# Kernel optimization log

Hardware: AMD Instinct MI355X
Metric: run time of the kernel (lower is better)

Reference implementation:

```python
import jax, jax.numpy as jnp
import numpy as np
import math

HID, NH, NKV, HD = 2048, 16, 4, 128
GROUPS = NH // NKV

def fq(x, bits, axis=None):
    # symmetric fake-quant with straight-through rounding; per-tensor unless axis given
    qmax = 2.0 ** (bits - 1) - 1.0
    if axis is None:
        amax = jnp.max(jnp.abs(x))
    else:
        amax = jnp.max(jnp.abs(x), axis=axis, keepdims=True)
    scale = jnp.maximum(amax, 1e-8) / qmax
    q = jnp.clip(jnp.round(x / scale), -qmax - 1.0, qmax) * scale
    return x + jax.lax.stop_gradient(q - x)

def dyn_quant_linear(x, W, b, w_bits=8):
    # DynamicQuantLinear: per-out-channel weight fake-quant + dynamic per-tensor 8-bit act quant
    Wq = fq(W, w_bits, axis=1)          # W: [out, in]
    xq = fq(x, 8)
    y = xq @ Wq.T
    return y + b if b is not None else y

def fq_matmul(a, b, a_bits, b_bits):
    # FakeQuantMatmul
    return jnp.einsum('hqd,hdk->hqk', fq(a, a_bits), fq(b, b_bits))

def rotate_half(x):
    x1, x2 = jnp.split(x, 2, axis=-1)
    return jnp.concatenate([-x2, x1], axis=-1)

def setup_inputs() -> dict:
    key = jax.random.key(0)
    ks = jax.random.split(key, 12)
    inp = {
        'hidden_states': jax.random.normal(ks[0], (1, 512, HID), jnp.float32),
        'cos': jax.random.uniform(ks[1], (1, 512, HD), jnp.float32),
        'sin': jax.random.uniform(ks[2], (1, 512, HD), jnp.float32),
        'cache_k': jax.random.normal(ks[3], (NKV, 8192, HD), jnp.float32),
        'cache_v': jax.random.normal(ks[4], (NKV, 8192, HD), jnp.float32),
        'mask': jnp.zeros((1, 512, 8192), jnp.float32),
        'Wq': jax.random.normal(ks[5], (NH * HD, HID), jnp.float32) * 0.02,
        'bq': jnp.zeros((NH * HD,), jnp.float32),
        'Wk': jax.random.normal(ks[6], (NKV * HD, HID), jnp.float32) * 0.02,
        'bk': jnp.zeros((NKV * HD,), jnp.float32),
        'Wv': jax.random.normal(ks[7], (NKV * HD, HID), jnp.float32) * 0.02,
        'bv': jnp.zeros((NKV * HD,), jnp.float32),
        'Wo': jax.random.normal(ks[8], (HID, NH * HD), jnp.float32) * 0.02,
    }
    return inp

def reference(hidden_states, cos, sin, cache_k, cache_v, mask, Wq, bq, Wk, bk, Wv, bv, Wo):
    # ConstFakeQuant on incoming caches
    cache_k = fq(cache_k, 8)
    cache_v = fq(cache_v, 8)
    seqlen = hidden_states.shape[1]
    x = hidden_states.reshape(seqlen, HID)  # batch_size == 1
    q = dyn_quant_linear(x, Wq, bq).reshape(seqlen, NH, HD).transpose(1, 0, 2)    # [NH,S,D]
    k = dyn_quant_linear(x, Wk, bk).reshape(seqlen, NKV, HD).transpose(1, 0, 2)   # [NKV,S,D]
    v = dyn_quant_linear(x, Wv, bv).reshape(seqlen, NKV, HD).transpose(1, 0, 2)   # [NKV,S,D]
    # RoPE
    q = q * cos + rotate_half(q) * sin
    k = k * cos + rotate_half(k) * sin
    c_len = cache_k.shape[1]
    # sliding KV cache: drop oldest seqlen, append new
    cache_k = jnp.concatenate([cache_k[:, seqlen:, :], k], axis=1)   # [NKV,c_len,D]
    cache_v = jnp.concatenate([cache_v[:, seqlen:, :], v], axis=1)
    kT = cache_k.transpose(0, 2, 1)                                   # [NKV,D,c_len]
    q4 = q.reshape(NKV, GROUPS * seqlen, HD)
    attn = fq_matmul(q4, kT, 8, 8)                                    # [NKV,G*S,c_len]
    attn = attn.reshape(NH, seqlen, c_len) / math.sqrt(HD)
    attn = attn + mask
    attn = jax.nn.softmax(attn, axis=-1)
    attn = attn.reshape(NKV, GROUPS * seqlen, c_len)
    out = fq_matmul(attn, cache_v, 8, 8)                              # sv: [NKV,G*S,D]
    out = out.reshape(NH, seqlen, HD).transpose(1, 0, 2).reshape(1, seqlen, HID)
    out = dyn_quant_linear(out.reshape(seqlen, HID), Wo, None).reshape(1, seqlen, HID)
    # cache outputs re-fake-quantized
    k_out = fq(k, 8)
    v_out = fq(v, 8)
    return (out, k_out, v_out)
```

## Files before the change

kernel.cpp:

```cpp
#include <hip/hip_runtime.h>
#include <math.h>

#define S_LEN 512
#define HID 2048
#define NH 16
#define NKV 4
#define HD 128
#define CL 8192
#define TAILN (CL - S_LEN)
#define KS1 16
#define KCH1 (CL / KS1)
#define KS2 8
#define KCH2 (CL / KS2)
#define INV_SQRT_HD 0.08838834764831845f

typedef unsigned short u16;
typedef __attribute__((ext_vector_type(8))) unsigned short u16x8;
typedef __attribute__((ext_vector_type(4))) unsigned short u16x4;
typedef __attribute__((ext_vector_type(8))) short bf16x8;
typedef __attribute__((ext_vector_type(4))) float f32x4;

enum {
  SC_AMAX_X = 0, SC_AMAX_CK, SC_AMAX_CK_TAIL, SC_AMAX_CV, SC_AMAX_CV_TAIL,
  SC_AMAX_Q, SC_AMAX_K, SC_AMAX_V, SC_AMAX_AO, SC_MIN_L,
  SC_NUM
};

__device__ __forceinline__ float warpMax64(float v) {
  #pragma unroll
  for (int o = 32; o; o >>= 1) v = fmaxf(v, __shfl_down(v, o, 64));
  return v;
}
__device__ __forceinline__ float warpMin64(float v) {
  #pragma unroll
  for (int o = 32; o; o >>= 1) v = fminf(v, __shfl_down(v, o, 64));
  return v;
}
__device__ __forceinline__ float blockMax256(float v) {
  __shared__ float sm_[4];
  __syncthreads();
  v = warpMax64(v);
  if ((threadIdx.x & 63) == 0) sm_[threadIdx.x >> 6] = v;
  __syncthreads();
  return fmaxf(fmaxf(sm_[0], sm_[1]), fmaxf(sm_[2], sm_[3]));
}
__device__ __forceinline__ float blockMin256(float v) {
  __shared__ float sn_[4];
  __syncthreads();
  v = warpMin64(v);
  if ((threadIdx.x & 63) == 0) sn_[threadIdx.x >> 6] = v;
  __syncthreads();
  return fminf(fminf(sn_[0], sn_[1]), fminf(sn_[2], sn_[3]));
}
__device__ __forceinline__ void atomicMinPosF(float* a, float v) {
  atomicMin((unsigned int*)a, __float_as_uint(v));
}
__device__ __forceinline__ float clampq(float q) {
  return fminf(fmaxf(q, -128.f), 127.f);
}
__device__ __forceinline__ u16 bf16bits(float f) {
  return (u16)(__float_as_uint(f) >> 16);
}
__device__ __forceinline__ float mk_scale(float am) {
  return fmaxf(am, 1e-8f) / 127.f;
}
__device__ __forceinline__ void gl2lds16(const u16* g, u16* l) {
  __builtin_amdgcn_global_load_lds((const __attribute__((address_space(1))) void*)g,
                                   (__attribute__((address_space(3))) void*)l, 16, 0, 0);
}

__global__ void k_init(float* sc) {
  int i = threadIdx.x;
  if (i < SC_NUM) sc[i] = (i == SC_MIN_L) ? INFINITY : 0.f;
}

__global__ __launch_bounds__(256) void k_absmax_part(const float* __restrict__ x, int n4,
                                                     float* __restrict__ pp) {
  float m = 0.f;
  const float4* x4 = (const float4*)x;
  for (int i = blockIdx.x * 256 + threadIdx.x; i < n4; i += gridDim.x * 256) {
    float4 v = x4[i];
    m = fmaxf(m, fmaxf(fmaxf(fabsf(v.x), fabsf(v.y)), fmaxf(fabsf(v.z), fabsf(v.w))));
  }
  m = blockMax256(m);
  if (threadIdx.x == 0) pp[blockIdx.x] = m;
}

__global__ __launch_bounds__(256) void k_absmax_caches_part(const float* __restrict__ ck,
                                                            const float* __restrict__ cv,
                                                            float* __restrict__ pp) {
  const int n4 = NKV * CL * HD / 4;
  float mkf = 0.f, mkt = 0.f, mvf = 0.f, mvt = 0.f;
  for (int i = blockIdx.x * 256 + threadIdx.x; i < 2 * n4; i += gridDim.x * 256) {
    int isv = i >= n4;
    int j = i - isv * n4;
    float4 v = ((const float4*)(isv ? cv : ck))[j];
    float a = fmaxf(fmaxf(fabsf(v.x), fabsf(v.y)), fmaxf(fabsf(v.z), fabsf(v.w)));
    int t = (j >> 5) & (CL - 1);
    if (isv) { mvf = fmaxf(mvf, a); if (t >= S_LEN) mvt = fmaxf(mvt, a); }
    else     { mkf = fmaxf(mkf, a); if (t >= S_LEN) mkt = fmaxf(mkt, a); }
  }
  mkf = blockMax256(mkf); mkt = blockMax256(mkt);
  mvf = blockMax256(mvf); mvt = blockMax256(mvt);
  if (threadIdx.x == 0) {
    pp[512 + blockIdx.x] = mkf;
    pp[1024 + blockIdx.x] = mkt;
    pp[1536 + blockIdx.x] = mvf;
    pp[2048 + blockIdx.x] = mvt;
  }
}

__global__ __launch_bounds__(256) void k_reduce_pre(const float* __restrict__ pp, float* __restrict__ sc) {
  const int slots[5] = {SC_AMAX_X, SC_AMAX_CK, SC_AMAX_CK_TAIL, SC_AMAX_CV, SC_AMAX_CV_TAIL};
  #pragma unroll
  for (int r = 0; r < 5; r++) {
    float v = fmaxf(pp[r * 512 + threadIdx.x], pp[r * 512 + 256 + threadIdx.x]);
    v = blockMax256(v);
    if (threadIdx.x == 0) sc[slots[r]] = v;
  }
}

__global__ __launch_bounds__(256) void k_quant_w_all(const float* __restrict__ Wq, const float* __restrict__ Wk,
                                                     const float* __restrict__ Wv, const float* __restrict__ Wo,
                                                     u16* __restrict__ WQb, u16* __restrict__ WKb,
                                                     u16* __restrict__ WVb, u16* __restrict__ WOb,
                                                     float* __restrict__ SWq, float* __restrict__ SWk,
                                                     float* __restrict__ SWv, float* __restrict__ SWo) {
  int r = blockIdx.x;
  const float* W; u16* Wb; float* SW; int row;
  if (r < 2048)      { W = Wq; Wb = WQb; SW = SWq; row = r; }
  else if (r < 2560) { W = Wk; Wb = WKb; SW = SWk; row = r - 2048; }
  else if (r < 3072) { W = Wv; Wb = WVb; SW = SWv; row = r - 2560; }
  else               { W = Wo; Wb = WOb; SW = SWo; row = r - 3072; }
  size_t base = (size_t)row * HID;
  const float4* w4 = (const float4*)(W + base);
  const int n4 = HID / 4;
  float am = 0.f;
  for (int i = threadIdx.x; i < n4; i += 256) {
    float4 v = w4[i];
    am = fmaxf(am, fmaxf(fmaxf(fabsf(v.x), fabsf(v.y)), fmaxf(fabsf(v.z), fabsf(v.w))));
  }
  am = blockMax256(am);
  float s = fmaxf(am, 1e-8f) / 127.f;
  if (threadIdx.x == 0) SW[row] = s;
  for (int i = threadIdx.x; i < n4; i += 256) {
    float4 v = w4[i];
    u16x4 o;
    o[0] = bf16bits(clampq(rintf(v.x / s)));
    o[1] = bf16bits(clampq(rintf(v.y / s)));
    o[2] = bf16bits(clampq(rintf(v.z / s)));
    o[3] = bf16bits(clampq(rintf(v.w / s)));
    *(u16x4*)(Wb + base + (size_t)i * 4) = o;
  }
}

__global__ __launch_bounds__(256) void k_quant_act_b(const float* __restrict__ in, u16* __restrict__ outp,
                                                     int n4, const float* __restrict__ sc, int axslot) {
  float s = mk_scale(sc[axslot]);
  const float4* i4 = (const float4*)in;
  for (int i = blockIdx.x * 256 + threadIdx.x; i < n4; i += gridDim.x * 256) {
    float4 v = i4[i];
    u16x4 o;
    o[0] = bf16bits(clampq(rintf(v.x / s)));
    o[1] = bf16bits(clampq(rintf(v.y / s)));
    o[2] = bf16bits(clampq(rintf(v.z / s)));
    o[3] = bf16bits(clampq(rintf(v.w / s)));
    *(u16x4*)(outp + (size_t)i * 4) = o;
  }
}

__global__ __launch_bounds__(256) void k_quant_q(const float* __restrict__ QB, u16* __restrict__ QI,
                                                 const float* __restrict__ sc) {
  int idx = blockIdx.x * 256 + threadIdx.x;
  float s = mk_scale(sc[SC_AMAX_Q]);
  int e = idx * 4;
  int srow = e >> 11, rem = e & 2047;
  int h = rem >> 7, d = rem & 127;
  float4 v = *(const float4*)&QB[e];
  u16x4 o;
  o[0] = bf16bits(clampq(rintf(v.x / s)));
  o[1] = bf16bits(clampq(rintf(v.y / s)));
  o[2] = bf16bits(clampq(rintf(v.z / s)));
  o[3] = bf16bits(clampq(rintf(v.w / s)));
  *(u16x4*)(QI + ((size_t)h * S_LEN + srow) * HD + d) = o;
}

__global__ __launch_bounds__(256) void k_gemm_qkv(const u16* __restrict__ A,
                                                  const u16* __restrict__ WQb, const u16* __restrict__ WKb,
                                                  const u16* __restrict__ WVb,
                                                  const float* __restrict__ SWq, const float* __restrict__ SWk,
                                                  const float* __restrict__ SWv,
                                                  const float* __restrict__ bq, const float* __restrict__ bk,
                                                  const float* __restrict__ bv,
                                                  const float* __restrict__ sc,
                                                  float* __restrict__ QB, float* __restrict__ KB,
                                                  float* __restrict__ VB) {
  __shared__ u16 Al[64 * 64];
  __shared__ u16 Bl[64 * 64];
  int bx = blockIdx.x;
  const u16* B; const float* SW; const float* bias; float* C; int N, c0;
  if (bx < 32)      { B = WQb; SW = SWq; bias = bq; C = QB; N = HID; c0 = bx * 64; }
  else if (bx < 40) { B = WKb; SW = SWk; bias = bk; C = KB; N = NKV * HD; c0 = (bx - 32) * 64; }
  else              { B = WVb; SW = SWv; bias = bv; C = VB; N = NKV * HD; c0 = (bx - 40) * 64; }
  int tid = threadIdx.x, lane = tid & 63, w = tid >> 6;
  int g = lane >> 4, c = lane & 15;
  int wy = w >> 1, wx = w & 1;
  int r0 = blockIdx.y * 64;
  float sx = mk_scale(sc[SC_AMAX_X]);
  f32x4 acc[2][2] = {};
  for (int k0 = 0; k0 < HID; k0 += 64) {
    __syncthreads();
    #pragma unroll
    for (int i = 0; i < 2; i++) {
      int b = tid + i * 256;
      int row = b >> 3, c8d = b & 7, c8s = c8d ^ (row & 7);
      gl2lds16(A + (size_t)(r0 + row) * HID + k0 + c8s * 8, Al + b * 8);
    }
    #pragma unroll
    for (int i = 0; i < 2; i++) {
      int b = tid + i * 256;
      int row = b >> 3, c8d = b & 7, c8s = c8d ^ (row & 7);
      gl2lds16(B + (size_t)(c0 + row) * HID + k0 + c8s * 8, Bl + b * 8);
    }
    __syncthreads();
    #pragma unroll
    for (int ks = 0; ks < 2; ks++) {
      bf16x8 af[2], bf[2];
      #pragma unroll
      for (int a = 0; a < 2; a++) {
        int row = wy * 32 + a * 16 + c;
        af[a] = *(const bf16x8*)(Al + row * 64 + (((4 * ks + g) ^ (row & 7)) * 8));
      }
      #pragma unroll
      for (int b = 0; b < 2; b++) {
        int row = wx * 32 + b * 16 + c;
        bf[b] = *(const bf16x8*)(Bl + row * 64 + (((4 * ks + g) ^ (row & 7)) * 8));
      }
      #pragma unroll
      for (int a = 0; a < 2; a++)
        #pragma unroll
        for (int b = 0; b < 2; b++)
          acc[a][b] = __builtin_amdgcn_mfma_f32_16x16x32_bf16(af[a], bf[b], acc[a][b], 0, 0, 0);
    }
  }
  #pragma unroll
  for (int a = 0; a < 2; a++)
    #pragma unroll
    for (int b = 0; b < 2; b++) {
      int col = c0 + wx * 32 + b * 16 + c;
      float sca = sx * SW[col];
      float bs = bias[col];
      #pragma unroll
      for (int r = 0; r < 4; r++) {
        int row = r0 + wy * 32 + a * 16 + 4 * g + r;
        C[(size_t)row * N + col] = acc[a][b][r] * sca + bs;
      }
    }
}

__global__ __launch_bounds__(256) void k_gemm_q(const u16* __restrict__ A, const u16* __restrict__ B,
                                                const float* __restrict__ SW, const float* __restrict__ sc,
                                                int axslot, float* __restrict__ C, int M, int N, int K) {
  __shared__ u16 Al[64 * 64];
  __shared__ u16 Bl[64 * 64];
  int tid = threadIdx.x, lane = tid & 63, w = tid >> 6;
  int g = lane >> 4, c = lane & 15;
  int wy = w >> 1, wx = w & 1;
  int r0 = blockIdx.y * 64, c0 = blockIdx.x * 64;
  float sx = mk_scale(sc[axslot]);
  f32x4 acc[2][2] = {};
  for (int k0 = 0; k0 < K; k0 += 64) {
    __syncthreads();
    #pragma unroll
    for (int i = 0; i < 2; i++) {
      int b = tid + i * 256;
      int row = b >> 3, c8d = b & 7, c8s = c8d ^ (row & 7);
      gl2lds16(A + (size_t)(r0 + row) * K + k0 + c8s * 8, Al + b * 8);
    }
    #pragma unroll
    for (int i = 0; i < 2; i++) {
      int b = tid + i * 256;
      int row = b >> 3, c8d = b & 7, c8s = c8d ^ (row & 7);
      gl2lds16(B + (size_t)(c0 + row) * K + k0 + c8s * 8, Bl + b * 8);
    }
    __syncthreads();
    #pragma unroll
    for (int ks = 0; ks < 2; ks++) {
      bf16x8 af[2], bf[2];
      #pragma unroll
      for (int a = 0; a < 2; a++) {
        int row = wy * 32 + a * 16 + c;
        af[a] = *(const bf16x8*)(Al + row * 64 + (((4 * ks + g) ^ (row & 7)) * 8));
      }
      #pragma unroll
      for (int b = 0; b < 2; b++) {
        int row = wx * 32 + b * 16 + c;
        bf[b] = *(const bf16x8*)(Bl + row * 64 + (((4 * ks + g) ^ (row & 7)) * 8));
      }
      #pragma unroll
      for (int a = 0; a < 2; a++)
        #pragma unroll
        for (int b = 0; b < 2; b++)
          acc[a][b] = __builtin_amdgcn_mfma_f32_16x16x32_bf16(af[a], bf[b], acc[a][b], 0, 0, 0);
    }
  }
  #pragma unroll
  for (int a = 0; a < 2; a++)
    #pragma unroll
    for (int b = 0; b < 2; b++) {
      int col = c0 + wx * 32 + b * 16 + c;
      float sca = sx * SW[col];
      #pragma unroll
      for (int r = 0; r < 4; r++) {
        int row = r0 + wy * 32 + a * 16 + 4 * g + r;
        C[(size_t)row * N + col] = acc[a][b][r] * sca;
      }
    }
}

__global__ __launch_bounds__(256) void k_rope_amax(float* __restrict__ QB, float* __restrict__ KB,
                                                   const float* __restrict__ VB,
                                                   const float* __restrict__ cosb, const float* __restrict__ sinb,
                                                   float* __restrict__ PR) {
  const int nQ = S_LEN * NH * 64;
  const int nK = S_LEN * NKV * 64;
  int idx = blockIdx.x * 256 + threadIdx.x;
  float am = 0.f;
  if (idx < nQ) {
    int s = idx >> 10, rem = idx & 1023, h = rem >> 6, d = rem & 63;
    float c1 = cosb[s * HD + d], s1 = sinb[s * HD + d];
    float c2 = cosb[s * HD + d + 64], s2 = sinb[s * HD + d + 64];
    float* p = &QB[(size_t)s * (NH * HD) + h * HD + d];
    float x1 = p[0], x2 = p[64];
    float y1 = x1 * c1 - x2 * s1;
    float y2 = x2 * c2 + x1 * s2;
    p[0] = y1; p[64] = y2;
    am = fmaxf(fabsf(y1), fabsf(y2));
  } else if (idx < nQ + nK) {
    int j = idx - nQ;
    int s = j >> 8, rem = j & 255, h = rem >> 6, d = rem & 63;
    float c1 = cosb[s * HD + d], s1 = sinb[s * HD + d];
    float c2 = cosb[s * HD + d + 64], s2 = sinb[s * HD + d + 64];
    float* p = &KB[(size_t)s * (NKV * HD) + h * HD + d];
    float x1 = p[0], x2 = p[64];
    float y1 = x1 * c1 - x2 * s1;
    float y2 = x2 * c2 + x1 * s2;
    p[0] = y1; p[64] = y2;
    am = fmaxf(fabsf(y1), fabsf(y2));
  } else {
    int j = idx - nQ - nK;
    float4 v = ((const float4*)VB)[j];
    am = fmaxf(fmaxf(fabsf(v.x), fabsf(v.y)), fmaxf(fabsf(v.z), fabsf(v.w)));
  }
  am = blockMax256(am);
  if (threadIdx.x == 0) PR[blockIdx.x] = am;
}

__global__ __launch_bounds__(256) void k_reduce_rope(const float* __restrict__ PR, float* __restrict__ sc) {
  float v = 0.f;
  #pragma unroll
  for (int i = 0; i < 8; i++) v = fmaxf(v, PR[threadIdx.x + 256 * i]);
  v = blockMax256(v);
  if (threadIdx.x == 0) sc[SC_AMAX_Q] = v;
  v = fmaxf(PR[2048 + threadIdx.x], PR[2048 + 256 + threadIdx.x]);
  v = blockMax256(v);
  if (threadIdx.x == 0) sc[SC_AMAX_K] = v;
  v = PR[2560 + threadIdx.x];
  v = blockMax256(v);
  if (threadIdx.x == 0) sc[SC_AMAX_V] = v;
}

__global__ __launch_bounds__(256) void k_build_cache_b(const float* __restrict__ ck, const float* __restrict__ cv,
                                                       const float* __restrict__ KB, const float* __restrict__ VB,
                                                       u16* __restrict__ KCb, u16* __restrict__ VCb,
                                                       float* __restrict__ dout, const float* __restrict__ sc) {
  const int n1 = NKV * CL * HD;
  const int nko = NKV * S_LEN * HD;
  const int total = 2 * n1 + 2 * nko;
  float sck = mk_scale(sc[SC_AMAX_CK]), scv = mk_scale(sc[SC_AMAX_CV]);
  float tqk = fminf(rintf(sc[SC_AMAX_CK_TAIL] / sck), 127.f) * sck;
  float tqv = fminf(rintf(sc[SC_AMAX_CV_TAIL] / scv), 127.f) * scv;
  float skn = fmaxf(fmaxf(tqk, sc[SC_AMAX_K]), 1e-8f) / 127.f;
  float svn = fmaxf(fmaxf(tqv, sc[SC_AMAX_V]), 1e-8f) / 127.f;
  float sko = mk_scale(sc[SC_AMAX_K]), svo = mk_scale(sc[SC_AMAX_V]);
  for (int i = blockIdx.x * 256 + threadIdx.x; i < total; i += gridDim.x * 256) {
    if (i < 2 * n1) {
      int isv = i >= n1;
      int j = i - isv * n1;
      int kvh = j / (CL * HD);
      int rem = j - kvh * CL * HD;
      int t = rem / HD, d = rem - t * HD;
      float s1 = isv ? scv : sck, s2 = isv ? svn : skn;
      float outi;
      if (t < TAILN) {
        float x = (isv ? cv : ck)[(size_t)kvh * CL * HD + (size_t)(t + S_LEN) * HD + d];
        float v1 = clampq(rintf(x / s1)) * s1;
        outi = clampq(rintf(v1 / s2));
      } else {
        float x = (isv ? VB : KB)[(size_t)(t - TAILN) * (NKV * HD) + kvh * HD + d];
        outi = clampq(rintf(x / s2));
      }
      (isv ? VCb : KCb)[j] = bf16bits(outi);
    } else {
      int j = i - 2 * n1;
      int isv = j >= nko;
      int j2 = j - isv * nko;
      int kvh = j2 / (S_LEN * HD);
      int rem = j2 - kvh * S_LEN * HD;
      int s = rem / HD, d = rem - s * HD;
      float x = (isv ? VB : KB)[(size_t)s * (NKV * HD) + kvh * HD + d];
      float ss = isv ? svo : sko;
      dout[(size_t)S_LEN * HID + j] = clampq(rintf(x / ss)) * ss;
    }
  }
}

__global__ __launch_bounds__(256) void k_transpose_v(const u16* __restrict__ VCb, u16* __restrict__ VT) {
  __shared__ u16 T[64][72];
  int bid = blockIdx.x;
  int kv = bid >> 8, rem = bid & 255, tb = rem >> 1, db = rem & 1;
  int tid = threadIdx.x;
  int r = tid >> 3, cb = tid & 7;
  #pragma unroll
  for (int i = 0; i < 2; i++) {
    int row = r + i * 32;
    u16x8 v = *(const u16x8*)(VCb + ((size_t)kv * CL + tb * 64 + row) * HD + db * 64 + cb * 8);
    *(u16x8*)&T[row][cb * 8] = v;
  }
  __syncthreads();
  #pragma unroll
  for (int i = 0; i < 2; i++) {
    int drow = r + i * 32;
    u16x8 v;
    #pragma unroll
    for (int j = 0; j < 8; j++) v[j] = T[cb * 8 + j][drow];
    *(u16x8*)(VT + ((size_t)kv * HD + db * 64 + drow) * CL + tb * 64 + cb * 8) = v;
  }
}

__global__ __launch_bounds__(256) void k_mattn1(const u16* __restrict__ QI, const u16* __restrict__ KCb,
                                                const float* __restrict__ mask, const float* __restrict__ sc,
                                                float* __restrict__ PM, float* __restrict__ PL) {
  __shared__ u16 Kl[64 * HD];
  int bid = blockIdx.x;
  int wki = (bid & 7) * (NH * 8 * KS1 / 8) + (bid >> 3);
  int kc = wki >> 7, rem2 = wki & 127, qb = rem2 >> 4, h = rem2 & 15, kv = h >> 2;
  int tid = threadIdx.x, lane = tid & 63, wv = tid >> 6, g = lane >> 4, c = lane & 15;
  float sq  = mk_scale(sc[SC_AMAX_Q]);
  float sck = mk_scale(sc[SC_AMAX_CK]);
  float tqk = fminf(rintf(sc[SC_AMAX_CK_TAIL] / sck), 127.f) * sck;
  float skn = fmaxf(fmaxf(tqk, sc[SC_AMAX_K]), 1e-8f) / 127.f;
  float sscale = sq * skn * INV_SQRT_HD;
  int q0 = qb * 64 + wv * 16;
  bf16x8 qf[4];
  {
    const u16* qrow = QI + ((size_t)h * S_LEN + q0 + c) * HD + g * 8;
    #pragma unroll
    for (int ds = 0; ds < 4; ds++) qf[ds] = *(const bf16x8*)(qrow + 32 * ds);
  }
  float m[4], l[4];
  #pragma unroll
  for (int r = 0; r < 4; r++) { m[r] = -INFINITY; l[r] = 0.f; }
  int qlane = q0 + 4 * g;
  int kbase0 = kc * KCH1;
  const u16* Kg = KCb + (size_t)kv * CL * HD;
  for (int kb = 0; kb < KCH1; kb += 64) {
    int kbase = kbase0 + kb;
    __syncthreads();
    #pragma unroll
    for (int i = 0; i < 4; i++) {
      int b = tid + i * 256;
      int row = b >> 4, c8d = b & 15, c8s = c8d ^ (row & 7);
      gl2lds16(Kg + (size_t)(kbase + row) * HD + c8s * 8, Kl + b * 8);
    }
    __syncthreads();
    f32x4 sc4[4];
    #pragma unroll
    for (int kf = 0; kf < 4; kf++) {
      f32x4 s4 = {0.f, 0.f, 0.f, 0.f};
      int krow = kf * 16 + c;
      #pragma unroll
      for (int ds = 0; ds < 4; ds++) {
        bf16x8 kf8 = *(const bf16x8*)(Kl + krow * HD + (((4 * ds + g) ^ (krow & 7)) * 8));
        s4 = __builtin_amdgcn_mfma_f32_16x16x32_bf16(qf[ds], kf8, s4, 0, 0, 0);
      }
      sc4[kf] = s4;
    }
    #pragma unroll
    for (int r = 0; r < 4; r++) {
      const float* mr = mask + (size_t)(qlane + r) * CL + kbase;
      float v0 = fmaf(sc4[0][r], sscale, mr[c]);
      float v1 = fmaf(sc4[1][r], sscale, mr[16 + c]);
      float v2 = fmaf(sc4[2][r], sscale, mr[32 + c]);
      float v3 = fmaf(sc4[3][r], sscale, mr[48 + c]);
      float tmax = fmaxf(fmaxf(v0, v1), fmaxf(v2, v3));
      float nm = fmaxf(m[r], tmax);
      float e0 = __expf(v0 - nm), e1 = __expf(v1 - nm);
      float e2 = __expf(v2 - nm), e3 = __expf(v3 - nm);
      float f = __expf(m[r] - nm);
      l[r] = fmaf(l[r], f, (e0 + e1) + (e2 + e3));
      m[r] = nm;
    }
  }
  #pragma unroll
  for (int r = 0; r < 4; r++) {
    #pragma unroll
    for (int off = 1; off < 16; off <<= 1) {
      float om = __shfl_xor(m[r], off, 64);
      float ol = __shfl_xor(l[r], off, 64);
      float nm = fmaxf(m[r], om);
      l[r] = l[r] * __expf(m[r] - nm) + ol * __expf(om - nm);
      m[r] = nm;
    }
  }
  if (c == 0) {
    size_t base = ((size_t)kc * NH + h) * S_LEN + qlane;
    #pragma unroll
    for (int r = 0; r < 4; r++) { PM[base + r] = m[r]; PL[base + r] = l[r]; }
  }
}

__global__ __launch_bounds__(256) void k_merge4(const float* __restrict__ PM, const float* __restrict__ PL,
                                                float* __restrict__ MLm, float* __restrict__ MLl, float* sc) {
  int idx = blockIdx.x * 256 + threadIdx.x;
  const int st = NH * S_LEN;
  float m = PM[idx];
  #pragma unroll
  for (int p = 1; p < KS1; p++) m = fmaxf(m, PM[p * st + idx]);
  float l = 0.f;
  #pragma unroll
  for (int p = 0; p < KS1; p++) l += PL[p * st + idx] * __expf(PM[p * st + idx] - m);
  MLm[idx] = m; MLl[idx] = l;
  float lm = blockMin256(l);
  if (threadIdx.x == 0) atomicMinPosF(&sc[SC_MIN_L], lm);
}

__global__ __launch_bounds__(256) void k_mattn2(const u16* __restrict__ QI, const u16* __restrict__ KCb,
                                                const u16* __restrict__ VT, const float* __restrict__ mask,
                                                const float* __restrict__ sc, const float* __restrict__ MLm,
                                                const float* __restrict__ MLl, float* __restrict__ AOp) {
  __shared__ u16 Kl[64 * HD];
  __shared__ u16 Vl[HD * 64];
  __shared__ u16 Pl[4 * 16 * 64];
  int bid = blockIdx.x;
  int wki = (bid & 7) * (NH * 8 * KS2 / 8) + (bid >> 3);
  int kc = wki >> 7, rem2 = wki & 127, qb = rem2 >> 4, h = rem2 & 15, kv = h >> 2;
  int tid = threadIdx.x, lane = tid & 63, wv = tid >> 6, g = lane >> 4, c = lane & 15;
  float sq  = mk_scale(sc[SC_AMAX_Q]);
  float sck = mk_scale(sc[SC_AMAX_CK]);
  float tqk = fminf(rintf(sc[SC_AMAX_CK_TAIL] / sck), 127.f) * sck;
  float skn = fmaxf(fmaxf(tqk, sc[SC_AMAX_K]), 1e-8f) / 127.f;
  float sscale = sq * skn * INV_SQRT_HD;
  float scv = mk_scale(sc[SC_AMAX_CV]);
  float tqv = fminf(rintf(sc[SC_AMAX_CV_TAIL] / scv), 127.f) * scv;
  float svn = fmaxf(fmaxf(tqv, sc[SC_AMAX_V]), 1e-8f) / 127.f;
  float sp  = mk_scale(1.0f / sc[SC_MIN_L]);
  float rsp = 1.0f / sp;
  float psv = sp * svn;
  int q0 = qb * 64 + wv * 16;
  bf16x8 qf[4];
  {
    const u16* qrow = QI + ((size_t)h * S_LEN + q0 + c) * HD + g * 8;
    #pragma unroll
    for (int ds = 0; ds < 4; ds++) qf[ds] = *(const bf16x8*)(qrow + 32 * ds);
  }
  int qlane = q0 + 4 * g;
  float mreg[4], invl[4];
  #pragma unroll
  for (int r = 0; r < 4; r++) {
    mreg[r] = MLm[h * S_LEN + qlane + r];
    invl[r] = 1.0f / MLl[h * S_LEN + qlane + r];
  }
  f32x4 acc[8] = {};
  const u16* Kg = KCb + (size_t)kv * CL * HD;
  const u16* Vg = VT + (size_t)kv * HD * CL;
  int kbase0 = kc * KCH2;
  u16* Pw = Pl + wv * 1024;
  for (int kb = 0; kb < KCH2; kb += 64) {
    int kbase = kbase0 + kb;
    __syncthreads();
    #pragma unroll
    for (int i = 0; i < 4; i++) {
      int b = tid + i * 256;
      int row = b >> 4, c8d = b & 15, c8s = c8d ^ (row & 7);
      gl2lds16(Kg + (size_t)(kbase + row) * HD + c8s * 8, Kl + b * 8);
    }
    #pragma unroll
    for (int i = 0; i < 4; i++) {
      int b = tid + i * 256;
      int row = b >> 3, c8d = b & 7, c8s = c8d ^ (row & 7);
      gl2lds16(Vg + (size_t)row * CL + kbase + c8s * 8, Vl + b * 8);
    }
    __syncthreads();
    #pragma unroll
    for (int kf = 0; kf < 4; kf++) {
      f32x4 s4 = {0.f, 0.f, 0.f, 0.f};
      int krow = kf * 16 + c;
      #pragma unroll
      for (int ds = 0; ds < 4; ds++) {
        bf16x8 kf8 = *(const bf16x8*)(Kl + krow * HD + (((4 * ds + g) ^ (krow & 7)) * 8));
        s4 = __builtin_amdgcn_mfma_f32_16x16x32_bf16(qf[ds], kf8, s4, 0, 0, 0);
      }
      int key = kbase + kf * 16 + c;
      #pragma unroll
      for (int r = 0; r < 4; r++) {
        float v = fmaf(s4[r], sscale, mask[(size_t)(qlane + r) * CL + key]);
        float p = __expf(v - mreg[r]) * invl[r];
        float pi = fminf(rintf(p * rsp), 127.f);
        int prow = 4 * g + r, pcol = kf * 16 + c;
        Pw[prow * 64 + (pcol ^ ((prow & 7) << 3))] = bf16bits(pi);
      }
    }
    asm volatile("s_waitcnt lgkmcnt(0)" ::: "memory");
    __builtin_amdgcn_sched_barrier(0);
    bf16x8 pa[2];
    #pragma unroll
    for (int s = 0; s < 2; s++)
      pa[s] = *(const bf16x8*)(Pw + c * 64 + ((32 * s + 8 * g) ^ ((c & 7) << 3)));
    #pragma unroll
    for (int dt = 0; dt < 8; dt++) {
      #pragma unroll
      for (int s = 0; s < 2; s++) {
        int drow = dt * 16 + c;
        bf16x8 vf = *(const bf16x8*)(Vl + drow * 64 + (((4 * s + g) ^ (drow & 7)) * 8));
        acc[dt] = __builtin_amdgcn_mfma_f32_16x16x32_bf16(pa[s], vf, acc[dt], 0, 0, 0);
      }
    }
  }
  float* outp = AOp + (size_t)kc * S_LEN * HID;
  #pragma unroll
  for (int dt = 0; dt < 8; dt++)
    #pragma unroll
    for (int r = 0; r < 4; r++)
      outp[(size_t)(qlane + r) * HID + h * HD + dt * 16 + c] = acc[dt][r] * psv;
}

__global__ __launch_bounds__(256) void k_combine_ao(const float* __restrict__ AOp, float* __restrict__ AO,
                                                    float* __restrict__ PA) {
  int idx = blockIdx.x * 256 + threadIdx.x;
  const int st = S_LEN * HID / 4;
  const f32x4* p4 = (const f32x4*)AOp;
  f32x4 a = p4[idx];
  #pragma unroll
  for (int p = 1; p < KS2; p++) {
    f32x4 b = p4[p * st + idx];
    a = a + b;
  }
  *((f32x4*)AO + idx) = a;
  float am = fmaxf(fmaxf(fabsf(a[0]), fabsf(a[1])), fmaxf(fabsf(a[2]), fabsf(a[3])));
  am = blockMax256(am);
  if (threadIdx.x == 0) PA[blockIdx.x] = am;
}

__global__ __launch_bounds__(256) void k_reduce_ao(const float* __restrict__ PA, float* __restrict__ sc) {
  float v = 0.f;
  #pragma unroll
  for (int i = 0; i < 4; i++) v = fmaxf(v, PA[threadIdx.x + 256 * i]);
  v = blockMax256(v);
  if (threadIdx.x == 0) sc[SC_AMAX_AO] = v;
}

extern "C" void kernel_launch(void* const* d_in, const int* in_sizes, int n_in,
                              void* d_out, int out_size, void* d_ws, size_t ws_size,
                              hipStream_t stream) {
  const float* hidden = (const float*)d_in[0];
  const float* cosb   = (const float*)d_in[1];
  const float* sinb   = (const float*)d_in[2];
  const float* cachek = (const float*)d_in[3];
  const float* cachev = (const float*)d_in[4];
  const float* mask   = (const float*)d_in[5];
  const float* Wq     = (const float*)d_in[6];
  const float* bq     = (const float*)d_in[7];
  const float* Wk     = (const float*)d_in[8];
  const float* bk     = (const float*)d_in[9];
  const float* Wv     = (const float*)d_in[10];
  const float* bv     = (const float*)d_in[11];
  const float* Wo     = (const float*)d_in[12];
  float* out = (float*)d_out;

  char* base = (char*)d_ws;
  auto alloc = [&](size_t bytes) { char* p = base; base += (bytes + 255) & ~(size_t)255; return p; };

  float* SC  = (float*)alloc(64 * 4);
  float* PP  = (float*)alloc(2560 * 4);
  float* PR  = (float*)alloc(2816 * 4);
  float* PA  = (float*)alloc(1024 * 4);
  float* SWq = (float*)alloc(HID * 4);
  float* SWk = (float*)alloc(NKV * HD * 4);
  float* SWv = (float*)alloc(NKV * HD * 4);
  float* SWo = (float*)alloc(HID * 4);
  u16* XI    = (u16*)alloc((size_t)S_LEN * HID * 2);
  u16* WQb   = (u16*)alloc((size_t)HID * HID * 2);
  u16* WKb   = (u16*)alloc((size_t)NKV * HD * HID * 2);
  u16* WVb   = (u16*)alloc((size_t)NKV * HD * HID * 2);
  u16* WOb   = (u16*)alloc((size_t)HID * HID * 2);
  float* QB  = (float*)alloc((size_t)S_LEN * HID * 4);
  float* KB  = (float*)alloc((size_t)S_LEN * NKV * HD * 4);
  float* VB  = (float*)alloc((size_t)S_LEN * NKV * HD * 4);
  u16* KCb   = (u16*)alloc((size_t)NKV * CL * HD * 2);
  u16* VCb   = (u16*)alloc((size_t)NKV * CL * HD * 2);
  u16* VT    = (u16*)alloc((size_t)NKV * HD * CL * 2);
  u16* QI    = (u16*)alloc((size_t)NH * S_LEN * HD * 2);
  float* PM  = (float*)alloc((size_t)KS1 * NH * S_LEN * 4);
  float* PL  = (float*)alloc((size_t)KS1 * NH * S_LEN * 4);
  float* MLm = (float*)alloc((size_t)NH * S_LEN * 4);
  float* MLl = (float*)alloc((size_t)NH * S_LEN * 4);
  float* AOp = (float*)alloc((size_t)KS2 * S_LEN * HID * 4);
  float* AO  = (float*)alloc((size_t)S_LEN * HID * 4);
  u16* AOi   = (u16*)alloc((size_t)S_LEN * HID * 2);

  k_init<<<1, 64, 0, stream>>>(SC);
  k_absmax_part<<<512, 256, 0, stream>>>(hidden, S_LEN * HID / 4, PP);
  k_absmax_caches_part<<<512, 256, 0, stream>>>(cachek, cachev, PP);
  k_reduce_pre<<<1, 256, 0, stream>>>(PP, SC);
  k_quant_w_all<<<5120, 256, 0, stream>>>(Wq, Wk, Wv, Wo, WQb, WKb, WVb, WOb, SWq, SWk, SWv, SWo);
  k_quant_act_b<<<1024, 256, 0, stream>>>(hidden, XI, S_LEN * HID / 4, SC, SC_AMAX_X);
  {
    dim3 g(48, S_LEN / 64);
    k_gemm_qkv<<<g, 256, 0, stream>>>(XI, WQb, WKb, WVb, SWq, SWk, SWv, bq, bk, bv, SC, QB, KB, VB);
  }
  k_rope_amax<<<2816, 256, 0, stream>>>(QB, KB, VB, cosb, sinb, PR);
  k_reduce_rope<<<1, 256, 0, stream>>>(PR, SC);
  k_build_cache_b<<<4096, 256, 0, stream>>>(cachek, cachev, KB, VB, KCb, VCb, out, SC);
  k_transpose_v<<<NKV * (CL / 64) * (HD / 64), 256, 0, stream>>>(VCb, VT);
  k_quant_q<<<1024, 256, 0, stream>>>(QB, QI, SC);
  k_mattn1<<<NH * 8 * KS1, 256, 0, stream>>>(QI, KCb, mask, SC, PM, PL);
  k_merge4<<<NH * S_LEN / 256, 256, 0, stream>>>(PM, PL, MLm, MLl, SC);
  k_mattn2<<<NH * 8 * KS2, 256, 0, stream>>>(QI, KCb, VT, mask, SC, MLm, MLl, AOp);
  k_combine_ao<<<1024, 256, 0, stream>>>(AOp, AO, PA);
  k_reduce_ao<<<1, 256, 0, stream>>>(PA, SC);
  k_quant_act_b<<<1024, 256, 0, stream>>>(AO, AOi, S_LEN * HID / 4, SC, SC_AMAX_AO);
  {
    dim3 g(HID / 64, S_LEN / 64);
    k_gemm_q<<<g, 256, 0, stream>>>(AOi, WOb, SWo, SC, SC_AMAX_AO, out, S_LEN, HID, HID);
  }
  (void)in_sizes; (void)n_in; (void)out_size; (void)ws_size;
}
```

Before: 234.1 us.

## Fuse prep kernels, fuse cache build with V transpose, widen attention wave tiles

Merges the init and the three absmax kernels into one launch, with the min-l init moved into the reduce kernel. Fuses KV cache quantization with the V transpose, using vectorized float4 loads and an LDS tile so the bf16 V cache is not re-read. Both attention kernels now run 128-thread blocks in which each wave handles 32 query rows, so each K/V fragment loaded from LDS feeds two MFMAs. This raises register pressure and halves the threads available to issue global-to-LDS loads per block.

```diff
diff --git a/kernel.cpp b/kernel.cpp
--- a/kernel.cpp
+++ b/kernel.cpp
@@ -8,6 +8,7 @@
 #define HD 128
 #define CL 8192
 #define TAILN (CL - S_LEN)
+#define NKO (NKV * S_LEN * HD)
 #define KS1 16
 #define KCH1 (CL / KS1)
 #define KS2 8
@@ -69,49 +70,45 @@
                                    (__attribute__((address_space(3))) void*)l, 16, 0, 0);
 }
 
-__global__ void k_init(float* sc) {
-  int i = threadIdx.x;
-  if (i < SC_NUM) sc[i] = (i == SC_MIN_L) ? INFINITY : 0.f;
-}
-
-__global__ __launch_bounds__(256) void k_absmax_part(const float* __restrict__ x, int n4,
-                                                     float* __restrict__ pp) {
-  float m = 0.f;
-  const float4* x4 = (const float4*)x;
-  for (int i = blockIdx.x * 256 + threadIdx.x; i < n4; i += gridDim.x * 256) {
-    float4 v = x4[i];
-    m = fmaxf(m, fmaxf(fmaxf(fabsf(v.x), fabsf(v.y)), fmaxf(fabsf(v.z), fabsf(v.w))));
-  }
-  m = blockMax256(m);
-  if (threadIdx.x == 0) pp[blockIdx.x] = m;
-}
-
-__global__ __launch_bounds__(256) void k_absmax_caches_part(const float* __restrict__ ck,
-                                                            const float* __restrict__ cv,
-                                                            float* __restrict__ pp) {
-  const int n4 = NKV * CL * HD / 4;
-  float mkf = 0.f, mkt = 0.f, mvf = 0.f, mvt = 0.f;
-  for (int i = blockIdx.x * 256 + threadIdx.x; i < 2 * n4; i += gridDim.x * 256) {
-    int isv = i >= n4;
-    int j = i - isv * n4;
-    float4 v = ((const float4*)(isv ? cv : ck))[j];
-    float a = fmaxf(fmaxf(fabsf(v.x), fabsf(v.y)), fmaxf(fabsf(v.z), fabsf(v.w)));
-    int t = (j >> 5) & (CL - 1);
-    if (isv) { mvf = fmaxf(mvf, a); if (t >= S_LEN) mvt = fmaxf(mvt, a); }
-    else     { mkf = fmaxf(mkf, a); if (t >= S_LEN) mkt = fmaxf(mkt, a); }
-  }
-  mkf = blockMax256(mkf); mkt = blockMax256(mkt);
-  mvf = blockMax256(mvf); mvt = blockMax256(mvt);
-  if (threadIdx.x == 0) {
-    pp[512 + blockIdx.x] = mkf;
-    pp[1024 + blockIdx.x] = mkt;
-    pp[1536 + blockIdx.x] = mvf;
-    pp[2048 + blockIdx.x] = mvt;
+__global__ __launch_bounds__(256) void k_pre(const float* __restrict__ hidden,
+                                             const float* __restrict__ ck, const float* __restrict__ cv,
+                                             float* __restrict__ pp) {
+  int b = blockIdx.x, tid = threadIdx.x;
+  if (b < 512) {
+    const int n4 = S_LEN * HID / 4;
+    float m = 0.f;
+    const float4* x4 = (const float4*)hidden;
+    for (int i = b * 256 + tid; i < n4; i += 512 * 256) {
+      float4 v = x4[i];
+      m = fmaxf(m, fmaxf(fmaxf(fabsf(v.x), fabsf(v.y)), fmaxf(fabsf(v.z), fabsf(v.w))));
+    }
+    m = blockMax256(m);
+    if (tid == 0) pp[b] = m;
+  } else {
+    int isv = b >= 1024;
+    int bb = b - (isv ? 1024 : 512);
+    const float4* x4 = (const float4*)(isv ? cv : ck);
+    const int n4 = NKV * CL * HD / 4;
+    float mf = 0.f, mt = 0.f;
+    for (int i = bb * 256 + tid; i < n4; i += 512 * 256) {
+      float4 v = x4[i];
+      float a = fmaxf(fmaxf(fabsf(v.x), fabsf(v.y)), fmaxf(fabsf(v.z), fabsf(v.w)));
+      mf = fmaxf(mf, a);
+      int t = (i >> 5) & (CL - 1);
+      if (t >= S_LEN) mt = fmaxf(mt, a);
+    }
+    mf = blockMax256(mf);
+    mt = blockMax256(mt);
+    if (tid == 0) {
+      pp[512 + isv * 1024 + bb] = mf;
+      pp[1024 + isv * 1024 + bb] = mt;
+    }
   }
 }
 
 __global__ __launch_bounds__(256) void k_reduce_pre(const float* __restrict__ pp, float* __restrict__ sc) {
   const int slots[5] = {SC_AMAX_X, SC_AMAX_CK, SC_AMAX_CK_TAIL, SC_AMAX_CV, SC_AMAX_CV_TAIL};
+  if (threadIdx.x == 0) sc[SC_MIN_L] = INFINITY;
   #pragma unroll
   for (int r = 0; r < 5; r++) {
     float v = fmaxf(pp[r * 512 + threadIdx.x], pp[r * 512 + 256 + threadIdx.x]);
@@ -370,75 +367,72 @@
   if (threadIdx.x == 0) sc[SC_AMAX_V] = v;
 }
 
-__global__ __launch_bounds__(256) void k_build_cache_b(const float* __restrict__ ck, const float* __restrict__ cv,
-                                                       const float* __restrict__ KB, const float* __restrict__ VB,
-                                                       u16* __restrict__ KCb, u16* __restrict__ VCb,
-                                                       float* __restrict__ dout, const float* __restrict__ sc) {
-  const int n1 = NKV * CL * HD;
-  const int nko = NKV * S_LEN * HD;
-  const int total = 2 * n1 + 2 * nko;
-  float sck = mk_scale(sc[SC_AMAX_CK]), scv = mk_scale(sc[SC_AMAX_CV]);
-  float tqk = fminf(rintf(sc[SC_AMAX_CK_TAIL] / sck), 127.f) * sck;
-  float tqv = fminf(rintf(sc[SC_AMAX_CV_TAIL] / scv), 127.f) * scv;
-  float skn = fmaxf(fmaxf(tqk, sc[SC_AMAX_K]), 1e-8f) / 127.f;
-  float svn = fmaxf(fmaxf(tqv, sc[SC_AMAX_V]), 1e-8f) / 127.f;
-  float sko = mk_scale(sc[SC_AMAX_K]), svo = mk_scale(sc[SC_AMAX_V]);
-  for (int i = blockIdx.x * 256 + threadIdx.x; i < total; i += gridDim.x * 256) {
-    if (i < 2 * n1) {
-      int isv = i >= n1;
-      int j = i - isv * n1;
-      int kvh = j / (CL * HD);
-      int rem = j - kvh * CL * HD;
-      int t = rem / HD, d = rem - t * HD;
-      float s1 = isv ? scv : sck, s2 = isv ? svn : skn;
-      float outi;
-      if (t < TAILN) {
-        float x = (isv ? cv : ck)[(size_t)kvh * CL * HD + (size_t)(t + S_LEN) * HD + d];
-        float v1 = clampq(rintf(x / s1)) * s1;
-        outi = clampq(rintf(v1 / s2));
-      } else {
-        float x = (isv ? VB : KB)[(size_t)(t - TAILN) * (NKV * HD) + kvh * HD + d];
-        outi = clampq(rintf(x / s2));
-      }
-      (isv ? VCb : KCb)[j] = bf16bits(outi);
+__global__ __launch_bounds__(256) void k_build_cache2(const float* __restrict__ ck, const float* __restrict__ cv,
+                                                      const float* __restrict__ KB, const float* __restrict__ VB,
+                                                      u16* __restrict__ KCb, u16* __restrict__ VCb,
+                                                      u16* __restrict__ VT, float* __restrict__ dout,
+                                                      const float* __restrict__ sc) {
+  __shared__ u16 T[64][140];
+  int b = blockIdx.x;
+  int isv = b >= NKV * 128;
+  int bb = b - isv * NKV * 128;
+  int kvh = bb >> 7, tb = bb & 127;
+  float s1 = mk_scale(sc[isv ? SC_AMAX_CV : SC_AMAX_CK]);
+  float tq = fminf(rintf(sc[isv ? SC_AMAX_CV_TAIL : SC_AMAX_CK_TAIL] / s1), 127.f) * s1;
+  float s2 = fmaxf(fmaxf(tq, sc[isv ? SC_AMAX_V : SC_AMAX_K]), 1e-8f) / 127.f;
+  float so = mk_scale(sc[isv ? SC_AMAX_V : SC_AMAX_K]);
+  const float* cache = isv ? cv : ck;
+  const float* fresh = isv ? VB : KB;
+  u16* Cb = isv ? VCb : KCb;
+  int tid = threadIdx.x;
+  int t0 = tb * 64;
+  #pragma unroll
+  for (int i = 0; i < 8; i++) {
+    int idx = tid + i * 256;
+    int t = idx >> 5, d4 = (idx & 31) << 2;
+    int tt = t0 + t;
+    float4 x;
+    float q0_, q1_, q2_, q3_;
+    if (tt < TAILN) {
+      x = *(const float4*)&cache[((size_t)kvh * CL + tt + S_LEN) * HD + d4];
+      q0_ = clampq(rintf(clampq(rintf(x.x / s1)) * s1 / s2));
+      q1_ = clampq(rintf(clampq(rintf(x.y / s1)) * s1 / s2));
+      q2_ = clampq(rintf(clampq(rintf(x.z / s1)) * s1 / s2));
+      q3_ = clampq(rintf(clampq(rintf(x.w / s1)) * s1 / s2));
     } else {
-      int j = i - 2 * n1;
-      int isv = j >= nko;
-      int j2 = j - isv * nko;
-      int kvh = j2 / (S_LEN * HD);
-      int rem = j2 - kvh * S_LEN * HD;
-      int s = rem / HD, d = rem - s * HD;
-      float x = (isv ? VB : KB)[(size_t)s * (NKV * HD) + kvh * HD + d];
-      float ss = isv ? svo : sko;
-      dout[(size_t)S_LEN * HID + j] = clampq(rintf(x / ss)) * ss;
-    }
-  }
-}
-
-__global__ __launch_bounds__(256) void k_transpose_v(const u16* __restrict__ VCb, u16* __restrict__ VT) {
-  __shared__ u16 T[64][72];
-  int bid = blockIdx.x;
-  int kv = bid >> 8, rem = bid & 255, tb = rem >> 1, db = rem & 1;
-  int tid = threadIdx.x;
-  int r = tid >> 3, cb = tid & 7;
-  #pragma unroll
-  for (int i = 0; i < 2; i++) {
-    int row = r + i * 32;
-    u16x8 v = *(const u16x8*)(VCb + ((size_t)kv * CL + tb * 64 + row) * HD + db * 64 + cb * 8);
-    *(u16x8*)&T[row][cb * 8] = v;
-  }
-  __syncthreads();
-  #pragma unroll
-  for (int i = 0; i < 2; i++) {
-    int drow = r + i * 32;
-    u16x8 v;
-    #pragma unroll
-    for (int j = 0; j < 8; j++) v[j] = T[cb * 8 + j][drow];
-    *(u16x8*)(VT + ((size_t)kv * HD + db * 64 + drow) * CL + tb * 64 + cb * 8) = v;
-  }
-}
-
-__global__ __launch_bounds__(256) void k_mattn1(const u16* __restrict__ QI, const u16* __restrict__ KCb,
+      x = *(const float4*)&fresh[(size_t)(tt - TAILN) * (NKV * HD) + kvh * HD + d4];
+      q0_ = clampq(rintf(x.x / s2));
+      q1_ = clampq(rintf(x.y / s2));
+      q2_ = clampq(rintf(x.z / s2));
+      q3_ = clampq(rintf(x.w / s2));
+      float4 o;
+      o.x = clampq(rintf(x.x / so)) * so;
+      o.y = clampq(rintf(x.y / so)) * so;
+      o.z = clampq(rintf(x.z / so)) * so;
+      o.w = clampq(rintf(x.w / so)) * so;
+      *(float4*)&dout[(size_t)S_LEN * HID + (size_t)isv * NKO +
+                      ((size_t)kvh * S_LEN + (tt - TAILN)) * HD + d4] = o;
+    }
+    u16x4 ov;
+    ov[0] = bf16bits(q0_); ov[1] = bf16bits(q1_); ov[2] = bf16bits(q2_); ov[3] = bf16bits(q3_);
+    *(u16x4*)(Cb + ((size_t)kvh * CL + tt) * HD + d4) = ov;
+    if (isv) *(u16x4*)&T[t][d4] = ov;
+  }
+  if (isv) {
+    __syncthreads();
+    #pragma unroll
+    for (int i = 0; i < 4; i++) {
+      int j = tid + i * 256;
+      int d = j >> 3, tc = (j & 7) << 3;
+      u16x8 v;
+      #pragma unroll
+      for (int k = 0; k < 8; k++) v[k] = T[tc + k][d];
+      *(u16x8*)(VT + ((size_t)kvh * HD + d) * CL + t0 + tc) = v;
+    }
+  }
+}
+
+__global__ __launch_bounds__(128) void k_mattn1(const u16* __restrict__ QI, const u16* __restrict__ KCb,
                                                 const float* __restrict__ mask, const float* __restrict__ sc,
                                                 float* __restrict__ PM, float* __restrict__ PL) {
   __shared__ u16 Kl[64 * HD];
@@ -451,72 +445,84 @@
   float tqk = fminf(rintf(sc[SC_AMAX_CK_TAIL] / sck), 127.f) * sck;
   float skn = fmaxf(fmaxf(tqk, sc[SC_AMAX_K]), 1e-8f) / 127.f;
   float sscale = sq * skn * INV_SQRT_HD;
-  int q0 = qb * 64 + wv * 16;
-  bf16x8 qf[4];
-  {
-    const u16* qrow = QI + ((size_t)h * S_LEN + q0 + c) * HD + g * 8;
-    #pragma unroll
-    for (int ds = 0; ds < 4; ds++) qf[ds] = *(const bf16x8*)(qrow + 32 * ds);
-  }
-  float m[4], l[4];
-  #pragma unroll
-  for (int r = 0; r < 4; r++) { m[r] = -INFINITY; l[r] = 0.f; }
-  int qlane = q0 + 4 * g;
+  int q0 = qb * 64 + wv * 32;
+  bf16x8 qf[2][4];
+  #pragma unroll
+  for (int u = 0; u < 2; u++) {
+    const u16* qrow = QI + ((size_t)h * S_LEN + q0 + 16 * u + c) * HD + g * 8;
+    #pragma unroll
+    for (int ds = 0; ds < 4; ds++) qf[u][ds] = *(const bf16x8*)(qrow + 32 * ds);
+  }
+  float m[2][4], l[2][4];
+  #pragma unroll
+  for (int u = 0; u < 2; u++)
+    #pragma unroll
+    for (int r = 0; r < 4; r++) { m[u][r] = -INFINITY; l[u][r] = 0.f; }
+  int qlane[2] = {q0 + 4 * g, q0 + 16 + 4 * g};
   int kbase0 = kc * KCH1;
   const u16* Kg = KCb + (size_t)kv * CL * HD;
   for (int kb = 0; kb < KCH1; kb += 64) {
     int kbase = kbase0 + kb;
     __syncthreads();
     #pragma unroll
-    for (int i = 0; i < 4; i++) {
-      int b = tid + i * 256;
+    for (int i = 0; i < 8; i++) {
+      int b = tid + i * 128;
       int row = b >> 4, c8d = b & 15, c8s = c8d ^ (row & 7);
       gl2lds16(Kg + (size_t)(kbase + row) * HD + c8s * 8, Kl + b * 8);
     }
     __syncthreads();
-    f32x4 sc4[4];
+    f32x4 sc4[4][2];
     #pragma unroll
     for (int kf = 0; kf < 4; kf++) {
-      f32x4 s4 = {0.f, 0.f, 0.f, 0.f};
+      sc4[kf][0] = (f32x4){0.f, 0.f, 0.f, 0.f};
+      sc4[kf][1] = (f32x4){0.f, 0.f, 0.f, 0.f};
       int krow = kf * 16 + c;
       #pragma unroll
       for (int ds = 0; ds < 4; ds++) {
         bf16x8 kf8 = *(const bf16x8*)(Kl + krow * HD + (((4 * ds + g) ^ (krow & 7)) * 8));
-        s4 = __builtin_amdgcn_mfma_f32_16x16x32_bf16(qf[ds], kf8, s4, 0, 0, 0);
-      }
-      sc4[kf] = s4;
-    }
+        #pragma unroll
+        for (int u = 0; u < 2; u++)
+          sc4[kf][u] = __builtin_amdgcn_mfma_f32_16x16x32_bf16(qf[u][ds], kf8, sc4[kf][u], 0, 0, 0);
+      }
+    }
+    #pragma unroll
+    for (int u = 0; u < 2; u++)
+      #pragma unroll
+      for (int r = 0; r < 4; r++) {
+        const float* mr = mask + (size_t)(qlane[u] + r) * CL + kbase;
+        float v0 = fmaf(sc4[0][u][r], sscale, mr[c]);
+        float v1 = fmaf(sc4[1][u][r], sscale, mr[16 + c]);
+        float v2 = fmaf(sc4[2][u][r], sscale, mr[32 + c]);
+        float v3 = fmaf(sc4[3][u][r], sscale, mr[48 + c]);
+        float tmax = fmaxf(fmaxf(v0, v1), fmaxf(v2, v3));
+        float nm = fmaxf(m[u][r], tmax);
+        float e0 = __expf(v0 - nm), e1 = __expf(v1 - nm);
+        float e2 = __expf(v2 - nm), e3 = __expf(v3 - nm);
+        float f = __expf(m[u][r] - nm);
+        l[u][r] = fmaf(l[u][r], f, (e0 + e1) + (e2 + e3));
+        m[u][r] = nm;
+      }
+  }
+  #pragma unroll
+  for (int u = 0; u < 2; u++)
     #pragma unroll
     for (int r = 0; r < 4; r++) {
-      const float* mr = mask + (size_t)(qlane + r) * CL + kbase;
-      float v0 = fmaf(sc4[0][r], sscale, mr[c]);
-      float v1 = fmaf(sc4[1][r], sscale, mr[16 + c]);
-      float v2 = fmaf(sc4[2][r], sscale, mr[32 + c]);
-      float v3 = fmaf(sc4[3][r], sscale, mr[48 + c]);
-      float tmax = fmaxf(fmaxf(v0, v1), fmaxf(v2, v3));
-      float nm = fmaxf(m[r], tmax);
-      float e0 = __expf(v0 - nm), e1 = __expf(v1 - nm);
-      float e2 = __expf(v2 - nm), e3 = __expf(v3 - nm);
-      float f = __expf(m[r] - nm);
-      l[r] = fmaf(l[r], f, (e0 + e1) + (e2 + e3));
-      m[r] = nm;
-    }
-  }
-  #pragma unroll
-  for (int r = 0; r < 4; r++) {
-    #pragma unroll
-    for (int off = 1; off < 16; off <<= 1) {
-      float om = __shfl_xor(m[r], off, 64);
-      float ol = __shfl_xor(l[r], off, 64);
-      float nm = fmaxf(m[r], om);
-      l[r] = l[r] * __expf(m[r] - nm) + ol * __expf(om - nm);
-      m[r] = nm;
-    }
-  }
+      #pragma unroll
+      for (int off = 1; off < 16; off <<= 1) {
+        float om = __shfl_xor(m[u][r], off, 64);
+        float ol = __shfl_xor(l[u][r], off, 64);
+        float nm = fmaxf(m[u][r], om);
+        l[u][r] = l[u][r] * __expf(m[u][r] - nm) + ol * __expf(om - nm);
+        m[u][r] = nm;
+      }
+    }
   if (c == 0) {
-    size_t base = ((size_t)kc * NH + h) * S_LEN + qlane;
-    #pragma unroll
-    for (int r = 0; r < 4; r++) { PM[base + r] = m[r]; PL[base + r] = l[r]; }
+    #pragma unroll
+    for (int u = 0; u < 2; u++) {
+      size_t base = ((size_t)kc * NH + h) * S_LEN + qlane[u];
+      #pragma unroll
+      for (int r = 0; r < 4; r++) { PM[base + r] = m[u][r]; PL[base + r] = l[u][r]; }
+    }
   }
 }
 
@@ -535,13 +541,13 @@
   if (threadIdx.x == 0) atomicMinPosF(&sc[SC_MIN_L], lm);
 }
 
-__global__ __launch_bounds__(256) void k_mattn2(const u16* __restrict__ QI, const u16* __restrict__ KCb,
+__global__ __launch_bounds__(128) void k_mattn2(const u16* __restrict__ QI, const u16* __restrict__ KCb,
                                                 const u16* __restrict__ VT, const float* __restrict__ mask,
                                                 const float* __restrict__ sc, const float* __restrict__ MLm,
                                                 const float* __restrict__ MLl, float* __restrict__ AOp) {
   __shared__ u16 Kl[64 * HD];
   __shared__ u16 Vl[HD * 64];
-  __shared__ u16 Pl[4 * 16 * 64];
+  __shared__ u16 Pl[2 * 32 * 64];
   int bid = blockIdx.x;
   int wki = (bid & 7) * (NH * 8 * KS2 / 8) + (bid >> 3);
   int kc = wki >> 7, rem2 = wki & 127, qb = rem2 >> 4, h = rem2 & 15, kv = h >> 2;
@@ -557,82 +563,97 @@
   float sp  = mk_scale(1.0f / sc[SC_MIN_L]);
   float rsp = 1.0f / sp;
   float psv = sp * svn;
-  int q0 = qb * 64 + wv * 16;
-  bf16x8 qf[4];
-  {
-    const u16* qrow = QI + ((size_t)h * S_LEN + q0 + c) * HD + g * 8;
-    #pragma unroll
-    for (int ds = 0; ds < 4; ds++) qf[ds] = *(const bf16x8*)(qrow + 32 * ds);
-  }
-  int qlane = q0 + 4 * g;
-  float mreg[4], invl[4];
-  #pragma unroll
-  for (int r = 0; r < 4; r++) {
-    mreg[r] = MLm[h * S_LEN + qlane + r];
-    invl[r] = 1.0f / MLl[h * S_LEN + qlane + r];
-  }
-  f32x4 acc[8] = {};
+  int q0 = qb * 64 + wv * 32;
+  bf16x8 qf[2][4];
+  #pragma unroll
+  for (int u = 0; u < 2; u++) {
+    const u16* qrow = QI + ((size_t)h * S_LEN + q0 + 16 * u + c) * HD + g * 8;
+    #pragma unroll
+    for (int ds = 0; ds < 4; ds++) qf[u][ds] = *(const bf16x8*)(qrow + 32 * ds);
+  }
+  int qlane[2] = {q0 + 4 * g, q0 + 16 + 4 * g};
+  float mreg[2][4], invl[2][4];
+  #pragma unroll
+  for (int u = 0; u < 2; u++)
+    #pragma unroll
+    for (int r = 0; r < 4; r++) {
+      mreg[u][r] = MLm[h * S_LEN + qlane[u] + r];
+      invl[u][r] = 1.0f / MLl[h * S_LEN + qlane[u] + r];
+    }
+  f32x4 acc[2][8] = {};
   const u16* Kg = KCb + (size_t)kv * CL * HD;
   const u16* Vg = VT + (size_t)kv * HD * CL;
   int kbase0 = kc * KCH2;
-  u16* Pw = Pl + wv * 1024;
+  u16* Pw = Pl + wv * 2048;
   for (int kb = 0; kb < KCH2; kb += 64) {
     int kbase = kbase0 + kb;
     __syncthreads();
     #pragma unroll
-    for (int i = 0; i < 4; i++) {
-      int b = tid + i * 256;
+    for (int i = 0; i < 8; i++) {
+      int b = tid + i * 128;
       int row = b >> 4, c8d = b & 15, c8s = c8d ^ (row & 7);
       gl2lds16(Kg + (size_t)(kbase + row) * HD + c8s * 8, Kl + b * 8);
     }
     #pragma unroll
-    for (int i = 0; i < 4; i++) {
-      int b = tid + i * 256;
+    for (int i = 0; i < 8; i++) {
+      int b = tid + i * 128;
       int row = b >> 3, c8d = b & 7, c8s = c8d ^ (row & 7);
       gl2lds16(Vg + (size_t)row * CL + kbase + c8s * 8, Vl + b * 8);
     }
     __syncthreads();
     #pragma unroll
     for (int kf = 0; kf < 4; kf++) {
-      f32x4 s4 = {0.f, 0.f, 0.f, 0.f};
+      f32x4 s4[2];
+      s4[0] = (f32x4){0.f, 0.f, 0.f, 0.f};
+      s4[1] = (f32x4){0.f, 0.f, 0.f, 0.f};
       int krow = kf * 16 + c;
       #pragma unroll
       for (int ds = 0; ds < 4; ds++) {
         bf16x8 kf8 = *(const bf16x8*)(Kl + krow * HD + (((4 * ds + g) ^ (krow & 7)) * 8));
-        s4 = __builtin_amdgcn_mfma_f32_16x16x32_bf16(qf[ds], kf8, s4, 0, 0, 0);
+        #pragma unroll
+        for (int u = 0; u < 2; u++)
+          s4[u] = __builtin_amdgcn_mfma_f32_16x16x32_bf16(qf[u][ds], kf8, s4[u], 0, 0, 0);
       }
       int key = kbase + kf * 16 + c;
       #pragma unroll
-      for (int r = 0; r < 4; r++) {
-        float v = fmaf(s4[r], sscale, mask[(size_t)(qlane + r) * CL + key]);
-        float p = __expf(v - mreg[r]) * invl[r];
-        float pi = fminf(rintf(p * rsp), 127.f);
-        int prow = 4 * g + r, pcol = kf * 16 + c;
-        Pw[prow * 64 + (pcol ^ ((prow & 7) << 3))] = bf16bits(pi);
-      }
+      for (int u = 0; u < 2; u++)
+        #pragma unroll
+        for (int r = 0; r < 4; r++) {
+          float v = fmaf(s4[u][r], sscale, mask[(size_t)(qlane[u] + r) * CL + key]);
+          float p = __expf(v - mreg[u][r]) * invl[u][r];
+          float pi = fminf(rintf(p * rsp), 127.f);
+          int prow = 16 * u + 4 * g + r;
+          Pw[prow * 64 + ((kf * 16 + c) ^ ((prow & 7) << 3))] = bf16bits(pi);
+        }
     }
     asm volatile("s_waitcnt lgkmcnt(0)" ::: "memory");
     __builtin_amdgcn_sched_barrier(0);
-    bf16x8 pa[2];
-    #pragma unroll
-    for (int s = 0; s < 2; s++)
-      pa[s] = *(const bf16x8*)(Pw + c * 64 + ((32 * s + 8 * g) ^ ((c & 7) << 3)));
+    bf16x8 pa[2][2];
+    #pragma unroll
+    for (int u = 0; u < 2; u++)
+      #pragma unroll
+      for (int s = 0; s < 2; s++)
+        pa[u][s] = *(const bf16x8*)(Pw + (16 * u + c) * 64 + ((32 * s + 8 * g) ^ ((c & 7) << 3)));
     #pragma unroll
     for (int dt = 0; dt < 8; dt++) {
       #pragma unroll
       for (int s = 0; s < 2; s++) {
         int drow = dt * 16 + c;
         bf16x8 vf = *(const bf16x8*)(Vl + drow * 64 + (((4 * s + g) ^ (drow & 7)) * 8));
-        acc[dt] = __builtin_amdgcn_mfma_f32_16x16x32_bf16(pa[s], vf, acc[dt], 0, 0, 0);
+        #pragma unroll
+        for (int u = 0; u < 2; u++)
+          acc[u][dt] = __builtin_amdgcn_mfma_f32_16x16x32_bf16(pa[u][s], vf, acc[u][dt], 0, 0, 0);
       }
     }
   }
   float* outp = AOp + (size_t)kc * S_LEN * HID;
   #pragma unroll
-  for (int dt = 0; dt < 8; dt++)
-    #pragma unroll
-    for (int r = 0; r < 4; r++)
-      outp[(size_t)(qlane + r) * HID + h * HD + dt * 16 + c] = acc[dt][r] * psv;
+  for (int u = 0; u < 2; u++)
+    #pragma unroll
+    for (int dt = 0; dt < 8; dt++)
+      #pragma unroll
+      for (int r = 0; r < 4; r++)
+        outp[(size_t)(qlane[u] + r) * HID + h * HD + dt * 16 + c] = acc[u][dt][r] * psv;
 }
 
 __global__ __launch_bounds__(256) void k_combine_ao(const float* __restrict__ AOp, float* __restrict__ AO,
@@ -709,9 +730,7 @@
   float* AO  = (float*)alloc((size_t)S_LEN * HID * 4);
   u16* AOi   = (u16*)alloc((size_t)S_LEN * HID * 2);
 
-  k_init<<<1, 64, 0, stream>>>(SC);
-  k_absmax_part<<<512, 256, 0, stream>>>(hidden, S_LEN * HID / 4, PP);
-  k_absmax_caches_part<<<512, 256, 0, stream>>>(cachek, cachev, PP);
+  k_pre<<<1536, 256, 0, stream>>>(hidden, cachek, cachev, PP);
   k_reduce_pre<<<1, 256, 0, stream>>>(PP, SC);
   k_quant_w_all<<<5120, 256, 0, stream>>>(Wq, Wk, Wv, Wo, WQb, WKb, WVb, WOb, SWq, SWk, SWv, SWo);
   k_quant_act_b<<<1024, 256, 0, stream>>>(hidden, XI, S_LEN * HID / 4, SC, SC_AMAX_X);
@@ -721,12 +740,11 @@
   }
   k_rope_amax<<<2816, 256, 0, stream>>>(QB, KB, VB, cosb, sinb, PR);
   k_reduce_rope<<<1, 256, 0, stream>>>(PR, SC);
-  k_build_cache_b<<<4096, 256, 0, stream>>>(cachek, cachev, KB, VB, KCb, VCb, out, SC);
-  k_transpose_v<<<NKV * (CL / 64) * (HD / 64), 256, 0, stream>>>(VCb, VT);
+  k_build_cache2<<<NKV * 128 * 2, 256, 0, stream>>>(cachek, cachev, KB, VB, KCb, VCb, VT, out, SC);
   k_quant_q<<<1024, 256, 0, stream>>>(QB, QI, SC);
-  k_mattn1<<<NH * 8 * KS1, 256, 0, stream>>>(QI, KCb, mask, SC, PM, PL);
+  k_mattn1<<<NH * 8 * KS1, 128, 0, stream>>>(QI, KCb, mask, SC, PM, PL);
   k_merge4<<<NH * S_LEN / 256, 256, 0, stream>>>(PM, PL, MLm, MLl, SC);
-  k_mattn2<<<NH * 8 * KS2, 256, 0, stream>>>(QI, KCb, VT, mask, SC, MLm, MLl, AOp);
+  k_mattn2<<<NH * 8 * KS2, 128, 0, stream>>>(QI, KCb, VT, mask, SC, MLm, MLl, AOp);
   k_combine_ao<<<1024, 256, 0, stream>>>(AOp, AO, PA);
   k_reduce_ao<<<1, 256, 0, stream>>>(PA, SC);
   k_quant_act_b<<<1024, 256, 0, stream>>>(AO, AOi, S_LEN * HID / 4, SC, SC_AMAX_AO);
```

New measurement: 391.7 us. 67.3% more time.
